# Optimization experiments

Measured on AMD Instinct MI355X. Metric: run time of the kernel, lower is better.

The kernel has to match this reference:

```python
import jax, jax.numpy as jnp
import numpy as np

N_NODES = 100000
N_EDGES = 3200000
IN_DIM = 512
OUT_DIM = 128


def setup_inputs() -> dict:
    key = jax.random.key(0)
    kx, kw, kr, kc, kv = jax.random.split(key, 5)
    x = jax.random.normal(kx, (N_NODES, IN_DIM), dtype=jnp.float32)
    # glorot uniform init for the weight, matching glorot_init in the source
    init_range = np.sqrt(6.0 / (IN_DIM + OUT_DIM)).astype(np.float32)
    W = jax.random.uniform(kw, (IN_DIM, OUT_DIM), dtype=jnp.float32,
                           minval=-init_range, maxval=init_range)
    edge_row = jax.random.randint(kr, (N_EDGES,), 0, N_NODES, dtype=jnp.int32)
    edge_col = jax.random.randint(kc, (N_EDGES,), 0, N_NODES, dtype=jnp.int32)
    edge_val = jax.random.uniform(kv, (N_EDGES,), dtype=jnp.float32)
    return {"x": x, "W": W, "edge_row": edge_row, "edge_col": edge_col,
            "edge_val": edge_val}


def reference(x, W, edge_row, edge_col, edge_val):
    # dense projection: [N, in] @ [in, out] -> [N, out]
    xp = x @ W
    # SpMM: out[r] += val * xp[c] for each edge (r, c, val)
    msgs = xp[edge_col] * edge_val[:, None]          # [E, out]
    agg = jax.ops.segment_sum(msgs, edge_row, num_segments=N_NODES)
    return jax.nn.relu(agg)
```

## Files before the change

kernel.cpp:

```cpp
#include <hip/hip_runtime.h>

#define M_NODES 100000
#define MPAD    100096
#define K_DIM   512
#define N_DIM   128
#define NUM_EDGES 3200000

#define RSHIFT  6
#define ROWS_PB 64
#define NBUCK   1563
#define BCAP    2432
#define EPW     4096
#define NAPPEND ((NUM_EDGES + EPW - 1) / EPW)

typedef __bf16 bf16x8 __attribute__((ext_vector_type(8)));
typedef float f32x16 __attribute__((ext_vector_type(16)));
typedef unsigned short ushort8 __attribute__((ext_vector_type(8)));
typedef unsigned short ushort4v __attribute__((ext_vector_type(4)));
typedef unsigned int uint32;

__device__ __forceinline__ unsigned short f2bf(float f) {
  uint32 u = __float_as_uint(f);
  u = (u + 0x7FFFu + ((u >> 16) & 1u)) >> 16;
  return (unsigned short)u;
}

__device__ __forceinline__ float bf_lo(uint32 m) {
  return __uint_as_float(m << 16);
}
__device__ __forceinline__ float bf_hi(uint32 m) {
  return __uint_as_float(m & 0xFFFF0000u);
}

__global__ __launch_bounds__(256) void wfrag_kernel(
    const float* __restrict__ W, unsigned short* __restrict__ Wf) {
  const int t = blockIdx.x * 256 + threadIdx.x;
  const int j = t & 7;
  const int lane = (t >> 3) & 63;
  const int ng = (t >> 9) & 3;
  const int ks = t >> 11;
  const int k = ks * 16 + ((lane >> 5) << 3) + j;
  const int n = (ng << 5) + (lane & 31);
  Wf[t] = f2bf(W[k * N_DIM + n]);
}

__global__ __launch_bounds__(256) void gemm_mfma_kernel(
    const float* __restrict__ x, const unsigned short* __restrict__ Wf,
    unsigned short* __restrict__ xp) {
  __shared__ unsigned short As[128][72];

  const int tid = threadIdx.x;
  const int w = tid >> 6;
  const int lane = tid & 63;
  const int l31 = lane & 31;
  const int lhi = lane >> 5;
  const int row0 = blockIdx.x * 128;

  f32x16 acc[4] = {};

  for (int k0 = 0; k0 < K_DIM; k0 += 64) {
#pragma unroll
    for (int it = 0; it < 8; ++it) {
      const int f = it * 256 + tid;
      const int r = f >> 4;
      const int kq = f & 15;
      int gr = row0 + r;
      if (gr >= M_NODES) gr = M_NODES - 1;
      const float4 v = *(const float4*)(x + (size_t)gr * K_DIM + k0 + kq * 4);
      ushort4v b = {f2bf(v.x), f2bf(v.y), f2bf(v.z), f2bf(v.w)};
      *(ushort4v*)(&As[r][kq * 4]) = b;
    }
    __syncthreads();

    const int ksg0 = k0 >> 4;
#pragma unroll
    for (int ks = 0; ks < 4; ++ks) {
      const bf16x8 a = __builtin_bit_cast(
          bf16x8, *(const ushort8*)(&As[w * 32 + l31][ks * 16 + lhi * 8]));
      const ushort8* bp =
          (const ushort8*)(Wf) + ((size_t)(ksg0 + ks) * 4 * 64 + lane);
#pragma unroll
      for (int ng = 0; ng < 4; ++ng) {
        const bf16x8 b = __builtin_bit_cast(bf16x8, bp[(size_t)ng * 64]);
        acc[ng] =
            __builtin_amdgcn_mfma_f32_32x32x16_bf16(a, b, acc[ng], 0, 0, 0);
      }
    }
    __syncthreads();
  }

  const int rbase = row0 + w * 32 + 4 * lhi;
#pragma unroll
  for (int ng = 0; ng < 4; ++ng) {
    const int cc = (ng << 5) + l31;
#pragma unroll
    for (int reg = 0; reg < 16; ++reg) {
      const int rr = rbase + (reg & 3) + 8 * (reg >> 2);
      xp[(size_t)rr * N_DIM + cc] = f2bf(acc[ng][reg]);
    }
  }
}

__device__ __forceinline__ int tag_edge(int r, int* lcnt) {
  const int b = r >> RSHIFT;
  const int s = atomicAdd(&lcnt[b], 1);
  return (b << 18) | (s << 6) | (r & (ROWS_PB - 1));
}

__device__ __forceinline__ void emit_edge(int p, int col, float v,
                                          const int* lbase,
                                          uint2* __restrict__ buckets) {
  const int b = (int)((unsigned)p >> 18);
  const int idx = lbase[b] + ((p >> 6) & 0xFFF);
  if (idx < BCAP)
    buckets[(size_t)b * BCAP + idx] = make_uint2(
        ((uint32)col << 6) | (uint32)(p & (ROWS_PB - 1)), __float_as_uint(v));
}

__global__ __launch_bounds__(256) void bin_append_kernel(
    const int* __restrict__ erow, const int* __restrict__ ecol,
    const float* __restrict__ eval, int* __restrict__ gcursor,
    uint2* __restrict__ buckets) {
  __shared__ int lcnt[NBUCK];
  __shared__ int lbase[NBUCK];
  const int tid = threadIdx.x;
  for (int i = tid; i < NBUCK; i += 256) lcnt[i] = 0;
  __syncthreads();

  const int base = blockIdx.x * EPW;
  int pk[16];
#pragma unroll
  for (int c = 0; c < 4; ++c) {
    const int e0 = base + c * 1024 + tid * 4;
    if (e0 < NUM_EDGES) {
      const int4 r4 = *(const int4*)(erow + e0);
      pk[c * 4 + 0] = tag_edge(r4.x, lcnt);
      pk[c * 4 + 1] = tag_edge(r4.y, lcnt);
      pk[c * 4 + 2] = tag_edge(r4.z, lcnt);
      pk[c * 4 + 3] = tag_edge(r4.w, lcnt);
    }
  }
  __syncthreads();

  for (int i = tid; i < NBUCK; i += 256) {
    const int c = lcnt[i];
    lbase[i] = c ? atomicAdd(&gcursor[i], c) : 0;
  }
  __syncthreads();

#pragma unroll
  for (int c = 0; c < 4; ++c) {
    const int e0 = base + c * 1024 + tid * 4;
    if (e0 < NUM_EDGES) {
      const int4 c4 = *(const int4*)(ecol + e0);
      const float4 v4 = *(const float4*)(eval + e0);
      emit_edge(pk[c * 4 + 0], c4.x, v4.x, lbase, buckets);
      emit_edge(pk[c * 4 + 1], c4.y, v4.y, lbase, buckets);
      emit_edge(pk[c * 4 + 2], c4.z, v4.z, lbase, buckets);
      emit_edge(pk[c * 4 + 3], c4.w, v4.w, lbase, buckets);
    }
  }
}

__global__ __launch_bounds__(256, 8) void bucket_gather_kernel(
    const unsigned short* __restrict__ xp, const int* __restrict__ gcursor,
    const uint2* __restrict__ buckets, float* __restrict__ out) {
  __shared__ uint2 eds[BCAP];
  __shared__ int rbase[ROWS_PB + 1];
  __shared__ int rcur[ROWS_PB];
  __shared__ int stmp[ROWS_PB];

  const int b = blockIdx.x;
  const int tid = threadIdx.x;
  int n = gcursor[b];
  if (n > BCAP) n = BCAP;

  if (tid < ROWS_PB) rcur[tid] = 0;
  __syncthreads();

  const uint2* bk = buckets + (size_t)b * BCAP;
  for (int i = tid; i < n; i += 256) atomicAdd(&rcur[bk[i].x & 63], 1);
  __syncthreads();

  if (tid < ROWS_PB) stmp[tid] = rcur[tid];
  __syncthreads();
  for (int off = 1; off < ROWS_PB; off <<= 1) {
    int v = 0, a = 0;
    if (tid < ROWS_PB) {
      v = stmp[tid];
      if (tid >= off) a = stmp[tid - off];
    }
    __syncthreads();
    if (tid < ROWS_PB) stmp[tid] = v + a;
    __syncthreads();
  }
  if (tid < ROWS_PB) {
    rbase[tid + 1] = stmp[tid];
    rcur[tid] = 0;
  }
  if (tid == 0) rbase[0] = 0;
  __syncthreads();

  for (int i = tid; i < n; i += 256) {
    const uint2 e = bk[i];
    const int rl = e.x & 63;
    const int pos = rbase[rl] + atomicAdd(&rcur[rl], 1);
    eds[pos] = e;
  }
  __syncthreads();

  const int wv = tid >> 6;
  const int lane = tid & 63;
  const uint32* xpl = (const uint32*)xp + lane;

  for (int rl = wv; rl < ROWS_PB; rl += 4) {
    const int row = (b << RSHIFT) + rl;
    if (row >= M_NODES) break;
    const int s = rbase[rl];
    const int e = rbase[rl + 1];

    float ax0 = 0.f, ay0 = 0.f, ax1 = 0.f, ay1 = 0.f;
    float ax2 = 0.f, ay2 = 0.f, ax3 = 0.f, ay3 = 0.f;
    int i = s;
    for (; i + 3 < e; i += 4) {
      const uint2 e0 = eds[i];
      const uint2 e1 = eds[i + 1];
      const uint2 e2 = eds[i + 2];
      const uint2 e3 = eds[i + 3];
      const uint32 m0 = xpl[(size_t)(e0.x >> 6) * 64];
      const uint32 m1 = xpl[(size_t)(e1.x >> 6) * 64];
      const uint32 m2 = xpl[(size_t)(e2.x >> 6) * 64];
      const uint32 m3 = xpl[(size_t)(e3.x >> 6) * 64];
      const float v0 = __uint_as_float(e0.y);
      const float v1 = __uint_as_float(e1.y);
      const float v2 = __uint_as_float(e2.y);
      const float v3 = __uint_as_float(e3.y);
      ax0 += v0 * bf_lo(m0); ay0 += v0 * bf_hi(m0);
      ax1 += v1 * bf_lo(m1); ay1 += v1 * bf_hi(m1);
      ax2 += v2 * bf_lo(m2); ay2 += v2 * bf_hi(m2);
      ax3 += v3 * bf_lo(m3); ay3 += v3 * bf_hi(m3);
    }
    for (; i < e; ++i) {
      const uint2 e0 = eds[i];
      const uint32 m0 = xpl[(size_t)(e0.x >> 6) * 64];
      const float v0 = __uint_as_float(e0.y);
      ax0 += v0 * bf_lo(m0);
      ay0 += v0 * bf_hi(m0);
    }

    float2 r;
    r.x = fmaxf((ax0 + ax1) + (ax2 + ax3), 0.f);
    r.y = fmaxf((ay0 + ay1) + (ay2 + ay3), 0.f);
    *(float2*)(out + (size_t)row * N_DIM + lane * 2) = r;
  }
}

extern "C" void kernel_launch(void* const* d_in, const int* in_sizes, int n_in,
                              void* d_out, int out_size, void* d_ws,
                              size_t ws_size, hipStream_t stream) {
  const float* x = (const float*)d_in[0];
  const float* W = (const float*)d_in[1];
  const int* erow = (const int*)d_in[2];
  const int* ecol = (const int*)d_in[3];
  const float* eval = (const float*)d_in[4];
  float* out = (float*)d_out;

  char* wsb = (char*)d_ws;
  size_t off = 0;
  auto alloc = [&](size_t bytes) {
    char* p = wsb + off;
    off = (off + bytes + 511) & ~(size_t)511;
    return p;
  };
  unsigned short* xp =
      (unsigned short*)alloc((size_t)MPAD * N_DIM * sizeof(unsigned short));
  unsigned short* Wf =
      (unsigned short*)alloc((size_t)K_DIM * N_DIM * sizeof(unsigned short));
  int* gcursor = (int*)alloc((size_t)NBUCK * sizeof(int));
  uint2* buckets = (uint2*)alloc((size_t)NBUCK * BCAP * sizeof(uint2));
  (void)ws_size;

  wfrag_kernel<<<(K_DIM * N_DIM) / 256, 256, 0, stream>>>(W, Wf);
  gemm_mfma_kernel<<<MPAD / 128, 256, 0, stream>>>(x, Wf, xp);

  hipMemsetAsync(gcursor, 0, (size_t)NBUCK * sizeof(int), stream);
  bin_append_kernel<<<NAPPEND, 256, 0, stream>>>(erow, ecol, eval, gcursor,
                                                 buckets);

  bucket_gather_kernel<<<NBUCK, 256, 0, stream>>>(xp, gcursor, buckets, out);
}
```

Baseline: 538.4 us.

## Fuse GEMM and edge binning into one launch, prefetch x tiles into registers

Merges the dense projection GEMM and the edge bucketing kernel into a single launch. Block index decides which role a block takes, and both roles share one static shared-memory buffer, so the bandwidth-bound binning can overlap the GEMM. The gcursor zeroing moves into the weight-fragment kernel, which removes a memset call. The GEMM also software-prefetches the next x tile into registers while the current tile is computed, at the cost of more registers per thread, which can reduce occupancy.

```diff
diff --git a/kernel.cpp b/kernel.cpp
--- a/kernel.cpp
+++ b/kernel.cpp
@@ -12,6 +12,7 @@
 #define BCAP    2432
 #define EPW     4096
 #define NAPPEND ((NUM_EDGES + EPW - 1) / EPW)
+#define GEMM_BLOCKS (MPAD / 128)
 
 typedef __bf16 bf16x8 __attribute__((ext_vector_type(8)));
 typedef float f32x16 __attribute__((ext_vector_type(16)));
@@ -33,7 +34,8 @@
 }
 
 __global__ __launch_bounds__(256) void wfrag_kernel(
-    const float* __restrict__ W, unsigned short* __restrict__ Wf) {
+    const float* __restrict__ W, unsigned short* __restrict__ Wf,
+    int* __restrict__ gcursor) {
   const int t = blockIdx.x * 256 + threadIdx.x;
   const int j = t & 7;
   const int lane = (t >> 3) & 63;
@@ -42,35 +44,51 @@
   const int k = ks * 16 + ((lane >> 5) << 3) + j;
   const int n = (ng << 5) + (lane & 31);
   Wf[t] = f2bf(W[k * N_DIM + n]);
-}
-
-__global__ __launch_bounds__(256) void gemm_mfma_kernel(
-    const float* __restrict__ x, const unsigned short* __restrict__ Wf,
-    unsigned short* __restrict__ xp) {
-  __shared__ unsigned short As[128][72];
+  if (t < NBUCK) gcursor[t] = 0;
+}
+
+__device__ __forceinline__ void gemm_body(int bx, char* smem,
+                                          const float* __restrict__ x,
+                                          const unsigned short* __restrict__ Wf,
+                                          unsigned short* __restrict__ xp) {
+  auto As = (unsigned short(*)[72])smem;
 
   const int tid = threadIdx.x;
   const int w = tid >> 6;
   const int lane = tid & 63;
   const int l31 = lane & 31;
   const int lhi = lane >> 5;
-  const int row0 = blockIdx.x * 128;
+  const int row0 = bx * 128;
 
   f32x16 acc[4] = {};
-
+  float4 rg[8];
+
+  auto load_tile = [&](int k0) {
+#pragma unroll
+    for (int it = 0; it < 8; ++it) {
+      const int fidx = it * 256 + tid;
+      const int rr = fidx >> 4;
+      const int kq = fidx & 15;
+      int gr = row0 + rr;
+      if (gr >= M_NODES) gr = M_NODES - 1;
+      rg[it] = *(const float4*)(x + (size_t)gr * K_DIM + k0 + kq * 4);
+    }
+  };
+
+  load_tile(0);
   for (int k0 = 0; k0 < K_DIM; k0 += 64) {
 #pragma unroll
     for (int it = 0; it < 8; ++it) {
-      const int f = it * 256 + tid;
-      const int r = f >> 4;
-      const int kq = f & 15;
-      int gr = row0 + r;
-      if (gr >= M_NODES) gr = M_NODES - 1;
-      const float4 v = *(const float4*)(x + (size_t)gr * K_DIM + k0 + kq * 4);
-      ushort4v b = {f2bf(v.x), f2bf(v.y), f2bf(v.z), f2bf(v.w)};
-      *(ushort4v*)(&As[r][kq * 4]) = b;
+      const int fidx = it * 256 + tid;
+      const int rr = fidx >> 4;
+      const int kq = fidx & 15;
+      ushort4v b = {f2bf(rg[it].x), f2bf(rg[it].y), f2bf(rg[it].z),
+                    f2bf(rg[it].w)};
+      *(ushort4v*)(&As[rr][kq * 4]) = b;
     }
     __syncthreads();
+
+    if (k0 + 64 < K_DIM) load_tile(k0 + 64);
 
     const int ksg0 = k0 >> 4;
 #pragma unroll
@@ -117,17 +135,19 @@
         ((uint32)col << 6) | (uint32)(p & (ROWS_PB - 1)), __float_as_uint(v));
 }
 
-__global__ __launch_bounds__(256) void bin_append_kernel(
-    const int* __restrict__ erow, const int* __restrict__ ecol,
-    const float* __restrict__ eval, int* __restrict__ gcursor,
-    uint2* __restrict__ buckets) {
-  __shared__ int lcnt[NBUCK];
-  __shared__ int lbase[NBUCK];
+__device__ __forceinline__ void bin_body(int bx, char* smem,
+                                         const int* __restrict__ erow,
+                                         const int* __restrict__ ecol,
+                                         const float* __restrict__ eval,
+                                         int* __restrict__ gcursor,
+                                         uint2* __restrict__ buckets) {
+  int* lcnt = (int*)smem;
+  int* lbase = (int*)(smem + 6912);
   const int tid = threadIdx.x;
   for (int i = tid; i < NBUCK; i += 256) lcnt[i] = 0;
   __syncthreads();
 
-  const int base = blockIdx.x * EPW;
+  const int base = bx * EPW;
   int pk[16];
 #pragma unroll
   for (int c = 0; c < 4; ++c) {
@@ -159,6 +179,20 @@
       emit_edge(pk[c * 4 + 2], c4.z, v4.z, lbase, buckets);
       emit_edge(pk[c * 4 + 3], c4.w, v4.w, lbase, buckets);
     }
+  }
+}
+
+__global__ __launch_bounds__(256) void gemm_bin_kernel(
+    const float* __restrict__ x, const unsigned short* __restrict__ Wf,
+    unsigned short* __restrict__ xp, const int* __restrict__ erow,
+    const int* __restrict__ ecol, const float* __restrict__ eval,
+    int* __restrict__ gcursor, uint2* __restrict__ buckets) {
+  __shared__ __align__(16) char smem[18432];
+  if (blockIdx.x < GEMM_BLOCKS) {
+    gemm_body(blockIdx.x, smem, x, Wf, xp);
+  } else {
+    bin_body(blockIdx.x - GEMM_BLOCKS, smem, erow, ecol, eval, gcursor,
+             buckets);
   }
 }
 
@@ -280,12 +314,10 @@
   uint2* buckets = (uint2*)alloc((size_t)NBUCK * BCAP * sizeof(uint2));
   (void)ws_size;
 
-  wfrag_kernel<<<(K_DIM * N_DIM) / 256, 256, 0, stream>>>(W, Wf);
-  gemm_mfma_kernel<<<MPAD / 128, 256, 0, stream>>>(x, Wf, xp);
-
-  hipMemsetAsync(gcursor, 0, (size_t)NBUCK * sizeof(int), stream);
-  bin_append_kernel<<<NAPPEND, 256, 0, stream>>>(erow, ecol, eval, gcursor,
-                                                 buckets);
+  wfrag_kernel<<<(K_DIM * N_DIM) / 256, 256, 0, stream>>>(W, Wf, gcursor);
+
+  gemm_bin_kernel<<<GEMM_BLOCKS + NAPPEND, 256, 0, stream>>>(
+      x, Wf, xp, erow, ecol, eval, gcursor, buckets);
 
   bucket_gather_kernel<<<NBUCK, 256, 0, stream>>>(xp, gcursor, buckets, out);
 }
```

New measurement: 496.7 us. -7.7%, faster.
